# Optimization experiments

Hardware: AMD Instinct MI355X
Metric: run time of the kernel (lower is better)

Reference implementation:

```python
import jax, jax.numpy as jnp
import numpy as np

B = 512            # num graphs
NPG = 128          # nodes per graph (== output_dim; required by masked_fill broadcast)
N = B * NPG        # 65536 total nodes
EPG = 1024         # edges per graph
E = B * EPG        # 524288 edges
IN_D, HID_D, OUT_D = 128, 128, 128
EPS = 1e-5         # BatchNorm1d default eps
NEG = -10000000000.0


def setup_inputs() -> dict:
    key = jax.random.key(0)
    k = jax.random.split(key, 16)
    x = jax.random.normal(k[0], (N, IN_D), dtype=jnp.float32)
    # intra-graph random edges (PyG Batch never has cross-graph edges)
    g = jnp.repeat(jnp.arange(B, dtype=jnp.int32), EPG)
    src = g * NPG + jax.random.randint(k[1], (E,), 0, NPG, dtype=jnp.int32)
    dst = g * NPG + jax.random.randint(k[2], (E,), 0, NPG, dtype=jnp.int32)
    edge_index = jnp.stack([src, dst])  # [2, E]
    batch = jnp.repeat(jnp.arange(B, dtype=jnp.int32), NPG)  # [N]

    def lin(kk, fi, fo):
        s = 1.0 / np.sqrt(fi)
        return jax.random.uniform(kk, (fi, fo), jnp.float32, -s, s)

    W1 = lin(k[3], IN_D, HID_D); b1 = jnp.zeros((HID_D,), jnp.float32)
    W2 = lin(k[4], HID_D, HID_D); b2 = jnp.zeros((HID_D,), jnp.float32)
    W3 = lin(k[5], HID_D, OUT_D); b3 = jnp.zeros((OUT_D,), jnp.float32)
    gamma1 = jnp.ones((HID_D,), jnp.float32); beta1 = jnp.zeros((HID_D,), jnp.float32)
    gamma2 = jnp.ones((HID_D,), jnp.float32); beta2 = jnp.zeros((HID_D,), jnp.float32)
    rm1 = 0.1 * jax.random.normal(k[6], (HID_D,), jnp.float32)
    rv1 = jax.random.uniform(k[7], (HID_D,), jnp.float32, 0.5, 1.5)
    rm2 = 0.1 * jax.random.normal(k[8], (HID_D,), jnp.float32)
    rv2 = jax.random.uniform(k[9], (HID_D,), jnp.float32, 0.5, 1.5)
    return dict(x=x, edge_index=edge_index, batch=batch,
                W1=W1, b1=b1, gamma1=gamma1, beta1=beta1, rm1=rm1, rv1=rv1,
                W2=W2, b2=b2, gamma2=gamma2, beta2=beta2, rm2=rm2, rv2=rv2,
                W3=W3, b3=b3)


def reference(x, edge_index, batch, W1, b1, gamma1, beta1, rm1, rv1,
              W2, b2, gamma2, beta2, rm2, rv2, W3, b3):
    src, dst = edge_index[0], edge_index[1]
    loops = jnp.arange(N, dtype=src.dtype)
    fs = jnp.concatenate([src, loops])  # sources with self-loops
    fd = jnp.concatenate([dst, loops])  # targets with self-loops
    deg = jax.ops.segment_sum(jnp.ones_like(fd, jnp.float32), fd, num_segments=N)
    dis = jnp.where(deg > 0, jax.lax.rsqrt(deg), 0.0)
    norm = dis[fs] * dis[fd]  # D^-1/2 A_hat D^-1/2 per edge

    def gcn(h, W, b):
        h = h @ W
        msg = h[fs] * norm[:, None]            # [E+N, d] gather
        return jax.ops.segment_sum(msg, fd, num_segments=N) + b  # scatter-add

    def bn(h, g, bt, rm, rv):  # BatchNorm1d in eval mode (running stats)
        return (h - rm) * jax.lax.rsqrt(rv + EPS) * g + bt

    h = jax.nn.relu(bn(gcn(x, W1, b1), gamma1, beta1, rm1, rv1))
    # dropout is a no-op in eval mode
    h = jax.nn.relu(bn(gcn(h, W2, b2), gamma2, beta2, rm2, rv2))
    h = gcn(h, W3, b3)

    # global mean pool (all graphs have exactly NPG nodes)
    pooled = jax.ops.segment_sum(h, batch, num_segments=B) / NPG  # [B, OUT_D]

    # vectorized get_visited_nodes_and_update_embeddings:
    # a node is 'connected' if it appears as src or dst of an edge of its graph;
    # the minimum connected node index of each graph is exempted.
    connected = jnp.zeros((N,), bool).at[src].set(True).at[dst].set(True)
    ids = jnp.arange(N, dtype=jnp.int32)
    cand = jnp.where(connected, ids, N)
    min_pg = jax.ops.segment_min(cand, batch, num_segments=B)  # [B]
    mask = connected & (ids != min_pg[batch])                  # [N]
    return jnp.where(mask.reshape(B, NPG), NEG, pooled)
```

## Files before the change

kernel.cpp:

```cpp
#include <hip/hip_runtime.h>
#include <hip/hip_bf16.h>


#define NGRAPH 512
#define EPG 1024
#define NEDGE (NGRAPH * EPG)
#define NEGV -10000000000.0f
#define LDS_MAIN 62468

typedef float f32x16 __attribute__((ext_vector_type(16)));
typedef float f32x4  __attribute__((ext_vector_type(4)));

#define MFMA8(a, b, c) __builtin_amdgcn_mfma_f32_32x32x16_fp8_fp8(a, b, c, 0, 0, 0)

__device__ unsigned char g_wf[32768];

__device__ __forceinline__ unsigned swz8(unsigned row, unsigned byte_in_row) {
  return ((row << 7) + byte_in_row) ^ ((row & 15u) << 3);
}

__device__ __forceinline__ unsigned pk4(float a, float b, float c, float d) {
  int r = __builtin_amdgcn_cvt_pk_fp8_f32(a, b, 0, false);
  r = __builtin_amdgcn_cvt_pk_fp8_f32(c, d, r, true);
  return (unsigned)r;
}

__global__ void prep_w(const float* __restrict__ W1, const float* __restrict__ W2) {
  int gid = blockIdx.x * 256 + threadIdx.x;
  int lyr = gid >> 11, r = gid & 2047;
  int lane = r & 63, ks = (r >> 6) & 7, nt = r >> 9;
  const float* W = lyr ? W2 : W1;
  int fo = nt * 32 + (lane & 31);
  int k0 = ks * 16 + (lane >> 5) * 8;
  uint2 o;
  o.x = pk4(W[(k0 + 0) * 128 + fo], W[(k0 + 1) * 128 + fo],
            W[(k0 + 2) * 128 + fo], W[(k0 + 3) * 128 + fo]);
  o.y = pk4(W[(k0 + 4) * 128 + fo], W[(k0 + 5) * 128 + fo],
            W[(k0 + 6) * 128 + fo], W[(k0 + 7) * 128 + fo]);
  ((uint2*)g_wf)[gid] = o;
}

__global__ __launch_bounds__(1024, 8) void gcn_all(
    const float* __restrict__ x, const int* __restrict__ ei,
    const float* __restrict__ b1v, const float* __restrict__ g1v,
    const float* __restrict__ be1v, const float* __restrict__ rm1v,
    const float* __restrict__ rv1v,
    const float* __restrict__ b2v, const float* __restrict__ g2v,
    const float* __restrict__ be2v, const float* __restrict__ rm2v,
    const float* __restrict__ rv2v,
    const float* __restrict__ W3g, const float* __restrict__ b3v,
    float* __restrict__ out) {
  extern __shared__ char sm[];
  char* AnB = sm;
  char* X0  = sm + 16384;
  char* Y0  = sm + 32768;
  unsigned* cntW  = (unsigned*)(sm + 49152);
  float*    dis   = (float*)(sm + 57344);
  unsigned* deg   = (unsigned*)(sm + 57856);
  unsigned* conn  = (unsigned*)(sm + 58368);
  float*    csumE = (float*)(sm + 58880);
  float*    scl1  = (float*)(sm + 59392);
  float*    shf1  = (float*)(sm + 59904);
  float*    scl2  = (float*)(sm + 60416);
  float*    shf2  = (float*)(sm + 60928);
  float*    vred  = (float*)(sm + 61440);
  float*    vout  = (float*)(sm + 61952);
  int*      minid = (int*)(sm + 62464);

  const int tid = threadIdx.x;
  const int g   = blockIdx.x;
  const int lane = tid & 63;
  const int wid  = tid >> 6;
  const int l31  = lane & 31;
  const int hi   = lane >> 5;
  const int mt   = wid >> 2;
  const int nt   = wid & 3;

  int es, ed;
  { int e = g * EPG + tid; es = ei[e] & 127; ed = ei[NEDGE + e] & 127; }
  const f32x4* xg = (const f32x4*)(x + (size_t)g * 128 * 128);
  f32x4 xr0 = xg[tid];
  f32x4 xr1 = xg[tid + 1024];
  f32x4 xr2 = xg[tid + 2048];
  f32x4 xr3 = xg[tid + 3072];

  ((uint2*)cntW)[tid] = make_uint2(0u, 0u);
  if (tid < 128) {
    deg[tid] = 1u; conn[tid] = 0u; csumE[tid] = 0.f;
    vred[tid] = 0.f; vout[tid] = 0.f;
    float s1 = rsqrtf(rv1v[tid] + 1e-5f) * g1v[tid];
    scl1[tid] = s1;
    shf1[tid] = be1v[tid] + (b1v[tid] - rm1v[tid]) * s1;
    float s2 = rsqrtf(rv2v[tid] + 1e-5f) * g2v[tid];
    scl2[tid] = s2;
    shf2[tid] = be2v[tid] + (b2v[tid] - rm2v[tid]) * s2;
  }
  if (tid == 0) *minid = 128;
  {
    int k0 = tid, k1 = tid + 1024, k2 = tid + 2048, k3 = tid + 3072;
    *(unsigned*)(Y0 + swz8(k0 >> 5, (k0 & 31) * 4)) =
        pk4(xr0[0], xr0[1], xr0[2], xr0[3]);
    *(unsigned*)(Y0 + swz8(k1 >> 5, (k1 & 31) * 4)) =
        pk4(xr1[0], xr1[1], xr1[2], xr1[3]);
    *(unsigned*)(Y0 + swz8(k2 >> 5, (k2 & 31) * 4)) =
        pk4(xr2[0], xr2[1], xr2[2], xr2[3]);
    *(unsigned*)(Y0 + swz8(k3 >> 5, (k3 & 31) * 4)) =
        pk4(xr3[0], xr3[1], xr3[2], xr3[3]);
  }
  __syncthreads();

  atomicAdd(&cntW[ed * 16 + (es >> 3)], 1u << (4 * (es & 7)));
  atomicAdd(&deg[ed], 1u);
  conn[es] = 1u;
  conn[ed] = 1u;
  {
    f32x16 a = {};
#pragma unroll
    for (int ks = 0; ks < 8; ++ks) {
      long af = *(const long*)(Y0 + swz8(mt * 32 + l31, ks * 16 + hi * 8));
      long bf = *(const long*)(g_wf + nt * 4096 + ks * 512 + lane * 8);
      a = MFMA8(af, bf, a);
    }
#pragma unroll
    for (int q = 0; q < 4; ++q)
      *(unsigned*)(X0 + swz8(nt * 32 + l31, mt * 32 + q * 8 + hi * 4)) =
          pk4(a[q * 4 + 0], a[q * 4 + 1], a[q * 4 + 2], a[q * 4 + 3]);
  }
  __syncthreads();

  {
    uint2 cw2 = ((const uint2*)cntW)[tid];
    int d = tid >> 3, q = tid & 7;
    float dd = rsqrtf((float)deg[d]);
    int sb = q * 16;
    uint4 dg0 = *(const uint4*)(deg + sb);
    uint4 dg1 = *(const uint4*)(deg + sb + 4);
    uint4 dg2 = *(const uint4*)(deg + sb + 8);
    uint4 dg3 = *(const uint4*)(deg + sb + 12);
    float ds16[16] = {
        rsqrtf((float)dg0.x), rsqrtf((float)dg0.y),
        rsqrtf((float)dg0.z), rsqrtf((float)dg0.w),
        rsqrtf((float)dg1.x), rsqrtf((float)dg1.y),
        rsqrtf((float)dg1.z), rsqrtf((float)dg1.w),
        rsqrtf((float)dg2.x), rsqrtf((float)dg2.y),
        rsqrtf((float)dg2.z), rsqrtf((float)dg2.w),
        rsqrtf((float)dg3.x), rsqrtf((float)dg3.y),
        rsqrtf((float)dg3.z), rsqrtf((float)dg3.w)};
#pragma unroll
    for (int hw = 0; hw < 2; ++hw) {
      int s0 = sb + hw * 8;
      unsigned w = hw ? cw2.y : cw2.x;
      float v[8];
#pragma unroll
      for (int i = 0; i < 8; ++i)
        v[i] = (float)((w >> (4 * i)) & 15u) * dd * ds16[hw * 8 + i];
      if (d >= s0 && d < s0 + 8) v[d - s0] += dd * dd;
      uint2 o;
      o.x = pk4(v[0], v[1], v[2], v[3]);
      o.y = pk4(v[4], v[5], v[6], v[7]);
      *(uint2*)(AnB + swz8(d, s0)) = o;
    }
  }
  atomicAdd(&csumE[es], rsqrtf((float)deg[es]) * rsqrtf((float)deg[ed]));
  if (tid < 128) {
    dis[tid] = rsqrtf((float)deg[tid]);
    if (conn[tid]) atomicMin(minid, tid);
  }
  __syncthreads();

  {
    f32x16 a = {};
#pragma unroll
    for (int ks = 0; ks < 8; ++ks) {
      long af = *(const long*)(X0 + swz8(mt * 32 + l31, ks * 16 + hi * 8));
      long bf = *(const long*)(AnB + swz8(nt * 32 + l31, ks * 16 + hi * 8));
      a = MFMA8(af, bf, a);
    }
    int d = nt * 32 + l31;
#pragma unroll
    for (int q = 0; q < 4; ++q) {
      int f0 = mt * 32 + q * 8 + hi * 4;
      f32x4 s4 = *(const f32x4*)(scl1 + f0);
      f32x4 h4 = *(const f32x4*)(shf1 + f0);
      *(unsigned*)(Y0 + swz8(d, f0)) =
          pk4(fmaxf(a[q * 4 + 0] * s4[0] + h4[0], 0.f),
              fmaxf(a[q * 4 + 1] * s4[1] + h4[1], 0.f),
              fmaxf(a[q * 4 + 2] * s4[2] + h4[2], 0.f),
              fmaxf(a[q * 4 + 3] * s4[3] + h4[3], 0.f));
    }
  }
  __syncthreads();

  {
    f32x16 a = {};
#pragma unroll
    for (int ks = 0; ks < 8; ++ks) {
      long af = *(const long*)(Y0 + swz8(mt * 32 + l31, ks * 16 + hi * 8));
      long bf = *(const long*)(g_wf + 16384 + nt * 4096 + ks * 512 + lane * 8);
      a = MFMA8(af, bf, a);
    }
#pragma unroll
    for (int q = 0; q < 4; ++q)
      *(unsigned*)(X0 + swz8(nt * 32 + l31, mt * 32 + q * 8 + hi * 4)) =
          pk4(a[q * 4 + 0], a[q * 4 + 1], a[q * 4 + 2], a[q * 4 + 3]);
  }
  __syncthreads();

  {
    f32x16 a = {};
#pragma unroll
    for (int ks = 0; ks < 8; ++ks) {
      long af = *(const long*)(X0 + swz8(mt * 32 + l31, ks * 16 + hi * 8));
      long bf = *(const long*)(AnB + swz8(nt * 32 + l31, ks * 16 + hi * 8));
      a = MFMA8(af, bf, a);
    }
    int n = nt * 32 + l31;
    float dv = dis[n];
    float cs = csumE[n] + dv * dv;
#pragma unroll
    for (int q = 0; q < 4; ++q) {
      int f0 = mt * 32 + q * 8 + hi * 4;
      f32x4 s4 = *(const f32x4*)(scl2 + f0);
      f32x4 h4 = *(const f32x4*)(shf2 + f0);
#pragma unroll
      for (int j = 0; j < 4; ++j) {
        float s = cs * fmaxf(a[q * 4 + j] * s4[j] + h4[j], 0.f);
        s += __shfl_xor(s, 1, 32);
        s += __shfl_xor(s, 2, 32);
        s += __shfl_xor(s, 4, 32);
        s += __shfl_xor(s, 8, 32);
        s += __shfl_xor(s, 16, 32);
        if (l31 == 0) atomicAdd(&vred[f0 + j], s);
      }
    }
  }
  __syncthreads();

  {
    int fo = tid & 127, part = tid >> 7;
    float a0 = 0.f;
#pragma unroll
    for (int i = 0; i < 16; ++i) {
      int fi = part * 16 + i;
      a0 += vred[fi] * W3g[fi * 128 + fo];
    }
    atomicAdd(&vout[fo], a0);
  }
  __syncthreads();

  if (tid < 128) {
    bool msk = (conn[tid] != 0u) && (tid != *minid);
    float val = vout[tid] * (1.0f / 128.0f) + b3v[tid];
    out[(size_t)g * 128 + tid] = msk ? NEGV : val;
  }
}

extern "C" void kernel_launch(void* const* d_in, const int* in_sizes, int n_in,
                              void* d_out, int out_size, void* d_ws, size_t ws_size,
                              hipStream_t stream) {
  (void)in_sizes; (void)n_in; (void)out_size; (void)d_ws; (void)ws_size;
  const float* x   = (const float*)d_in[0];
  const int*   ei  = (const int*)d_in[1];
  const float* W1  = (const float*)d_in[3];
  const float* b1  = (const float*)d_in[4];
  const float* g1  = (const float*)d_in[5];
  const float* be1 = (const float*)d_in[6];
  const float* rm1 = (const float*)d_in[7];
  const float* rv1 = (const float*)d_in[8];
  const float* W2  = (const float*)d_in[9];
  const float* b2  = (const float*)d_in[10];
  const float* g2  = (const float*)d_in[11];
  const float* be2 = (const float*)d_in[12];
  const float* rm2 = (const float*)d_in[13];
  const float* rv2 = (const float*)d_in[14];
  const float* W3  = (const float*)d_in[15];
  const float* b3  = (const float*)d_in[16];

  prep_w<<<dim3(16), dim3(256), 0, stream>>>(W1, W2);
  gcn_all<<<dim3(NGRAPH), dim3(1024), LDS_MAIN, stream>>>(
      x, ei, b1, g1, be1, rm1, rv1, b2, g2, be2, rm2, rv2, W3, b3,
      (float*)d_out);
}
```

Before: 37.63 us.

## Halve block size to 512 threads with two MFMA N-tiles per wave

The fused GCN kernel now runs 512 threads per graph instead of 1024. Each wave computes two 32x32 output tiles that share the A fragments, and each thread handles two edges and eight x rows, with fragments preloaded into registers ahead of the MFMA chains. The goal is more work per wave, A-fragment reuse, and more instruction-level parallelism with fewer waves syncing at each barrier. In exchange, per-thread register pressure rises and the launch bound drops to 4 blocks of 512 threads, which may reduce occupancy or latency hiding.

Measured after the change: 33.96 us. 1.11x faster.

```diff
diff --git a/kernel.cpp b/kernel.cpp
--- a/kernel.cpp
+++ b/kernel.cpp
@@ -40,7 +40,7 @@
   ((uint2*)g_wf)[gid] = o;
 }
 
-__global__ __launch_bounds__(1024, 8) void gcn_all(
+__global__ __launch_bounds__(512, 4) void gcn_all(
     const float* __restrict__ x, const int* __restrict__ ei,
     const float* __restrict__ b1v, const float* __restrict__ g1v,
     const float* __restrict__ be1v, const float* __restrict__ rm1v,
@@ -52,8 +52,8 @@
     float* __restrict__ out) {
   extern __shared__ char sm[];
   char* AnB = sm;
-  char* X0  = sm + 16384;
-  char* Y0  = sm + 32768;
+  char* Y0  = sm + 16384;
+  char* X0  = sm + 32768;
   unsigned* cntW  = (unsigned*)(sm + 49152);
   float*    dis   = (float*)(sm + 57344);
   unsigned* deg   = (unsigned*)(sm + 57856);
@@ -73,18 +73,25 @@
   const int wid  = tid >> 6;
   const int l31  = lane & 31;
   const int hi   = lane >> 5;
-  const int mt   = wid >> 2;
-  const int nt   = wid & 3;
-
-  int es, ed;
-  { int e = g * EPG + tid; es = ei[e] & 127; ed = ei[NEDGE + e] & 127; }
+  const int mt   = wid >> 1;
+  const int nt0  = (wid & 1) * 2;
+
+  int es[2], ed[2];
+#pragma unroll
+  for (int j = 0; j < 2; ++j) {
+    int e = g * EPG + tid + 512 * j;
+    es[j] = ei[e] & 127;
+    ed[j] = ei[NEDGE + e] & 127;
+  }
   const f32x4* xg = (const f32x4*)(x + (size_t)g * 128 * 128);
-  f32x4 xr0 = xg[tid];
-  f32x4 xr1 = xg[tid + 1024];
-  f32x4 xr2 = xg[tid + 2048];
-  f32x4 xr3 = xg[tid + 3072];
-
-  ((uint2*)cntW)[tid] = make_uint2(0u, 0u);
+  f32x4 xr[8];
+#pragma unroll
+  for (int j = 0; j < 8; ++j) xr[j] = xg[tid + 512 * j];
+
+  {
+    uint4 z; z.x = 0; z.y = 0; z.z = 0; z.w = 0;
+    ((uint4*)cntW)[tid] = z;
+  }
   if (tid < 128) {
     deg[tid] = 1u; conn[tid] = 0u; csumE[tid] = 0.f;
     vred[tid] = 0.f; vout[tid] = 0.f;
@@ -96,64 +103,69 @@
     shf2[tid] = be2v[tid] + (b2v[tid] - rm2v[tid]) * s2;
   }
   if (tid == 0) *minid = 128;
-  {
-    int k0 = tid, k1 = tid + 1024, k2 = tid + 2048, k3 = tid + 3072;
-    *(unsigned*)(Y0 + swz8(k0 >> 5, (k0 & 31) * 4)) =
-        pk4(xr0[0], xr0[1], xr0[2], xr0[3]);
-    *(unsigned*)(Y0 + swz8(k1 >> 5, (k1 & 31) * 4)) =
-        pk4(xr1[0], xr1[1], xr1[2], xr1[3]);
-    *(unsigned*)(Y0 + swz8(k2 >> 5, (k2 & 31) * 4)) =
-        pk4(xr2[0], xr2[1], xr2[2], xr2[3]);
-    *(unsigned*)(Y0 + swz8(k3 >> 5, (k3 & 31) * 4)) =
-        pk4(xr3[0], xr3[1], xr3[2], xr3[3]);
-  }
-  __syncthreads();
-
-  atomicAdd(&cntW[ed * 16 + (es >> 3)], 1u << (4 * (es & 7)));
-  atomicAdd(&deg[ed], 1u);
-  conn[es] = 1u;
-  conn[ed] = 1u;
-  {
-    f32x16 a = {};
-#pragma unroll
-    for (int ks = 0; ks < 8; ++ks) {
-      long af = *(const long*)(Y0 + swz8(mt * 32 + l31, ks * 16 + hi * 8));
-      long bf = *(const long*)(g_wf + nt * 4096 + ks * 512 + lane * 8);
-      a = MFMA8(af, bf, a);
-    }
-#pragma unroll
-    for (int q = 0; q < 4; ++q)
-      *(unsigned*)(X0 + swz8(nt * 32 + l31, mt * 32 + q * 8 + hi * 4)) =
-          pk4(a[q * 4 + 0], a[q * 4 + 1], a[q * 4 + 2], a[q * 4 + 3]);
-  }
-  __syncthreads();
-
-  {
-    uint2 cw2 = ((const uint2*)cntW)[tid];
-    int d = tid >> 3, q = tid & 7;
+#pragma unroll
+  for (int j = 0; j < 8; ++j) {
+    int k = tid + 512 * j;
+    *(unsigned*)(Y0 + swz8(k >> 5, (k & 31) * 4)) =
+        pk4(xr[j][0], xr[j][1], xr[j][2], xr[j][3]);
+  }
+  __syncthreads();
+
+  {
+    long wb0[8], wb1[8];
+#pragma unroll
+    for (int ks = 0; ks < 8; ++ks) {
+      wb0[ks] = *(const long*)(g_wf + (nt0 + 0) * 4096 + ks * 512 + lane * 8);
+      wb1[ks] = *(const long*)(g_wf + (nt0 + 1) * 4096 + ks * 512 + lane * 8);
+    }
+#pragma unroll
+    for (int j = 0; j < 2; ++j) {
+      atomicAdd(&cntW[ed[j] * 16 + (es[j] >> 3)], 1u << (4 * (es[j] & 7)));
+      atomicAdd(&deg[ed[j]], 1u);
+      conn[es[j]] = 1u;
+      conn[ed[j]] = 1u;
+    }
+    long af[8];
+#pragma unroll
+    for (int ks = 0; ks < 8; ++ks)
+      af[ks] = *(const long*)(Y0 + swz8(mt * 32 + l31, ks * 16 + hi * 8));
+    f32x16 c0 = {}, c1 = {};
+#pragma unroll
+    for (int ks = 0; ks < 8; ++ks) {
+      c0 = MFMA8(af[ks], wb0[ks], c0);
+      c1 = MFMA8(af[ks], wb1[ks], c1);
+    }
+#pragma unroll
+    for (int n = 0; n < 2; ++n) {
+      int f = (nt0 + n) * 32 + l31;
+      const f32x16& c = n ? c1 : c0;
+#pragma unroll
+      for (int q = 0; q < 4; ++q)
+        *(unsigned*)(X0 + swz8(f, mt * 32 + q * 8 + hi * 4)) =
+            pk4(c[q * 4 + 0], c[q * 4 + 1], c[q * 4 + 2], c[q * 4 + 3]);
+    }
+  }
+  __syncthreads();
+
+  {
+    uint4 cw = ((const uint4*)cntW)[tid];
+    int d = tid >> 2, q4 = tid & 3;
     float dd = rsqrtf((float)deg[d]);
-    int sb = q * 16;
-    uint4 dg0 = *(const uint4*)(deg + sb);
-    uint4 dg1 = *(const uint4*)(deg + sb + 4);
-    uint4 dg2 = *(const uint4*)(deg + sb + 8);
-    uint4 dg3 = *(const uint4*)(deg + sb + 12);
-    float ds16[16] = {
-        rsqrtf((float)dg0.x), rsqrtf((float)dg0.y),
-        rsqrtf((float)dg0.z), rsqrtf((float)dg0.w),
-        rsqrtf((float)dg1.x), rsqrtf((float)dg1.y),
-        rsqrtf((float)dg1.z), rsqrtf((float)dg1.w),
-        rsqrtf((float)dg2.x), rsqrtf((float)dg2.y),
-        rsqrtf((float)dg2.z), rsqrtf((float)dg2.w),
-        rsqrtf((float)dg3.x), rsqrtf((float)dg3.y),
-        rsqrtf((float)dg3.z), rsqrtf((float)dg3.w)};
-#pragma unroll
-    for (int hw = 0; hw < 2; ++hw) {
-      int s0 = sb + hw * 8;
-      unsigned w = hw ? cw2.y : cw2.x;
+    unsigned w4[4] = {cw.x, cw.y, cw.z, cw.w};
+#pragma unroll
+    for (int j = 0; j < 4; ++j) {
+      int s0 = q4 * 32 + j * 8;
+      uint4 dg0 = *(const uint4*)(deg + s0);
+      uint4 dg1 = *(const uint4*)(deg + s0 + 4);
+      float ds8[8] = {rsqrtf((float)dg0.x), rsqrtf((float)dg0.y),
+                      rsqrtf((float)dg0.z), rsqrtf((float)dg0.w),
+                      rsqrtf((float)dg1.x), rsqrtf((float)dg1.y),
+                      rsqrtf((float)dg1.z), rsqrtf((float)dg1.w)};
+      unsigned w = w4[j];
       float v[8];
 #pragma unroll
       for (int i = 0; i < 8; ++i)
-        v[i] = (float)((w >> (4 * i)) & 15u) * dd * ds16[hw * 8 + i];
+        v[i] = (float)((w >> (4 * i)) & 15u) * dd * ds8[i];
       if (d >= s0 && d < s0 + 8) v[d - s0] += dd * dd;
       uint2 o;
       o.x = pk4(v[0], v[1], v[2], v[3]);
@@ -161,7 +173,10 @@
       *(uint2*)(AnB + swz8(d, s0)) = o;
     }
   }
-  atomicAdd(&csumE[es], rsqrtf((float)deg[es]) * rsqrtf((float)deg[ed]));
+#pragma unroll
+  for (int j = 0; j < 2; ++j)
+    atomicAdd(&csumE[es[j]],
+              rsqrtf((float)deg[es[j]]) * rsqrtf((float)deg[ed[j]]));
   if (tid < 128) {
     dis[tid] = rsqrtf((float)deg[tid]);
     if (conn[tid]) atomicMin(minid, tid);
@@ -169,54 +184,85 @@
   __syncthreads();
 
   {
-    f32x16 a = {};
-#pragma unroll
-    for (int ks = 0; ks < 8; ++ks) {
-      long af = *(const long*)(X0 + swz8(mt * 32 + l31, ks * 16 + hi * 8));
-      long bf = *(const long*)(AnB + swz8(nt * 32 + l31, ks * 16 + hi * 8));
-      a = MFMA8(af, bf, a);
-    }
-    int d = nt * 32 + l31;
-#pragma unroll
-    for (int q = 0; q < 4; ++q) {
-      int f0 = mt * 32 + q * 8 + hi * 4;
-      f32x4 s4 = *(const f32x4*)(scl1 + f0);
-      f32x4 h4 = *(const f32x4*)(shf1 + f0);
-      *(unsigned*)(Y0 + swz8(d, f0)) =
-          pk4(fmaxf(a[q * 4 + 0] * s4[0] + h4[0], 0.f),
-              fmaxf(a[q * 4 + 1] * s4[1] + h4[1], 0.f),
-              fmaxf(a[q * 4 + 2] * s4[2] + h4[2], 0.f),
-              fmaxf(a[q * 4 + 3] * s4[3] + h4[3], 0.f));
-    }
-  }
-  __syncthreads();
-
-  {
-    f32x16 a = {};
-#pragma unroll
-    for (int ks = 0; ks < 8; ++ks) {
-      long af = *(const long*)(Y0 + swz8(mt * 32 + l31, ks * 16 + hi * 8));
-      long bf = *(const long*)(g_wf + 16384 + nt * 4096 + ks * 512 + lane * 8);
-      a = MFMA8(af, bf, a);
-    }
-#pragma unroll
-    for (int q = 0; q < 4; ++q)
-      *(unsigned*)(X0 + swz8(nt * 32 + l31, mt * 32 + q * 8 + hi * 4)) =
-          pk4(a[q * 4 + 0], a[q * 4 + 1], a[q * 4 + 2], a[q * 4 + 3]);
-  }
-  __syncthreads();
-
-  {
-    f32x16 a = {};
-#pragma unroll
-    for (int ks = 0; ks < 8; ++ks) {
-      long af = *(const long*)(X0 + swz8(mt * 32 + l31, ks * 16 + hi * 8));
-      long bf = *(const long*)(AnB + swz8(nt * 32 + l31, ks * 16 + hi * 8));
-      a = MFMA8(af, bf, a);
-    }
-    int n = nt * 32 + l31;
-    float dv = dis[n];
-    float cs = csumE[n] + dv * dv;
+    long af[8], b0[8], b1[8];
+#pragma unroll
+    for (int ks = 0; ks < 8; ++ks) {
+      af[ks] = *(const long*)(X0 + swz8(mt * 32 + l31, ks * 16 + hi * 8));
+      b0[ks] = *(const long*)(AnB + swz8((nt0 + 0) * 32 + l31, ks * 16 + hi * 8));
+      b1[ks] = *(const long*)(AnB + swz8((nt0 + 1) * 32 + l31, ks * 16 + hi * 8));
+    }
+    f32x16 c0 = {}, c1 = {};
+#pragma unroll
+    for (int ks = 0; ks < 8; ++ks) {
+      c0 = MFMA8(af[ks], b0[ks], c0);
+      c1 = MFMA8(af[ks], b1[ks], c1);
+    }
+#pragma unroll
+    for (int n = 0; n < 2; ++n) {
+      int d = (nt0 + n) * 32 + l31;
+      const f32x16& c = n ? c1 : c0;
+#pragma unroll
+      for (int q = 0; q < 4; ++q) {
+        int f0 = mt * 32 + q * 8 + hi * 4;
+        f32x4 s4 = *(const f32x4*)(scl1 + f0);
+        f32x4 h4 = *(const f32x4*)(shf1 + f0);
+        *(unsigned*)(Y0 + swz8(d, f0)) =
+            pk4(fmaxf(c[q * 4 + 0] * s4[0] + h4[0], 0.f),
+                fmaxf(c[q * 4 + 1] * s4[1] + h4[1], 0.f),
+                fmaxf(c[q * 4 + 2] * s4[2] + h4[2], 0.f),
+                fmaxf(c[q * 4 + 3] * s4[3] + h4[3], 0.f));
+      }
+    }
+  }
+  __syncthreads();
+
+  {
+    long wb0[8], wb1[8];
+#pragma unroll
+    for (int ks = 0; ks < 8; ++ks) {
+      wb0[ks] = *(const long*)(g_wf + 16384 + (nt0 + 0) * 4096 + ks * 512 + lane * 8);
+      wb1[ks] = *(const long*)(g_wf + 16384 + (nt0 + 1) * 4096 + ks * 512 + lane * 8);
+    }
+    long af[8];
+#pragma unroll
+    for (int ks = 0; ks < 8; ++ks)
+      af[ks] = *(const long*)(Y0 + swz8(mt * 32 + l31, ks * 16 + hi * 8));
+    f32x16 c0 = {}, c1 = {};
+#pragma unroll
+    for (int ks = 0; ks < 8; ++ks) {
+      c0 = MFMA8(af[ks], wb0[ks], c0);
+      c1 = MFMA8(af[ks], wb1[ks], c1);
+    }
+#pragma unroll
+    for (int n = 0; n < 2; ++n) {
+      int f = (nt0 + n) * 32 + l31;
+      const f32x16& c = n ? c1 : c0;
+#pragma unroll
+      for (int q = 0; q < 4; ++q)
+        *(unsigned*)(X0 + swz8(f, mt * 32 + q * 8 + hi * 4)) =
+            pk4(c[q * 4 + 0], c[q * 4 + 1], c[q * 4 + 2], c[q * 4 + 3]);
+    }
+  }
+  __syncthreads();
+
+  {
+    long af[8], b0[8], b1[8];
+#pragma unroll
+    for (int ks = 0; ks < 8; ++ks) {
+      af[ks] = *(const long*)(X0 + swz8(mt * 32 + l31, ks * 16 + hi * 8));
+      b0[ks] = *(const long*)(AnB + swz8((nt0 + 0) * 32 + l31, ks * 16 + hi * 8));
+      b1[ks] = *(const long*)(AnB + swz8((nt0 + 1) * 32 + l31, ks * 16 + hi * 8));
+    }
+    f32x16 c0 = {}, c1 = {};
+#pragma unroll
+    for (int ks = 0; ks < 8; ++ks) {
+      c0 = MFMA8(af[ks], b0[ks], c0);
+      c1 = MFMA8(af[ks], b1[ks], c1);
+    }
+    int nA = (nt0 + 0) * 32 + l31, nB = (nt0 + 1) * 32 + l31;
+    float dvA = dis[nA], dvB = dis[nB];
+    float csA = csumE[nA] + dvA * dvA;
+    float csB = csumE[nB] + dvB * dvB;
 #pragma unroll
     for (int q = 0; q < 4; ++q) {
       int f0 = mt * 32 + q * 8 + hi * 4;
@@ -224,7 +270,8 @@
       f32x4 h4 = *(const f32x4*)(shf2 + f0);
 #pragma unroll
       for (int j = 0; j < 4; ++j) {
-        float s = cs * fmaxf(a[q * 4 + j] * s4[j] + h4[j], 0.f);
+        float s = csA * fmaxf(c0[q * 4 + j] * s4[j] + h4[j], 0.f) +
+                  csB * fmaxf(c1[q * 4 + j] * s4[j] + h4[j], 0.f);
         s += __shfl_xor(s, 1, 32);
         s += __shfl_xor(s, 2, 32);
         s += __shfl_xor(s, 4, 32);
@@ -240,8 +287,8 @@
     int fo = tid & 127, part = tid >> 7;
     float a0 = 0.f;
 #pragma unroll
-    for (int i = 0; i < 16; ++i) {
-      int fi = part * 16 + i;
+    for (int i = 0; i < 32; ++i) {
+      int fi = part * 32 + i;
       a0 += vred[fi] * W3g[fi * 128 + fo];
     }
     atomicAdd(&vout[fo], a0);
@@ -277,7 +324,7 @@
   const float* b3  = (const float*)d_in[16];
 
   prep_w<<<dim3(16), dim3(256), 0, stream>>>(W1, W2);
-  gcn_all<<<dim3(NGRAPH), dim3(1024), LDS_MAIN, stream>>>(
+  gcn_all<<<dim3(NGRAPH), dim3(512), LDS_MAIN, stream>>>(
       x, ei, b1, g1, be1, rm1, rv1, b2, g2, be2, rm2, rv2, W3, b3,
       (float*)d_out);
 }
```
